# Kernel tuning notes

Measured on AMD Instinct MI355X. Metric: run time of the kernel, lower is better.

Reference implementation:

```python
import jax, jax.numpy as jnp
import numpy as np

N_NODES = 100000


def gin_layer(x, src, dst, W, b):
    # GINConv with Linear nn, eps=0: Linear(x + sum_{j in N(i)} x_j)
    agg = jax.ops.segment_sum(x[src], dst, num_segments=N_NODES)  # [N, d]
    return (x + agg) @ W + b


def setup_inputs() -> dict:
    key = jax.random.key(0)
    ks = jax.random.split(key, 8)
    in_c, hid, out_c = 128, 128, 64
    x = jax.random.normal(ks[0], (N_NODES, in_c), dtype=jnp.float32)
    edge_index = jax.random.randint(ks[1], (2, 600000), 0, N_NODES, dtype=jnp.int64)
    def lin(k, fan_in, fan_out):
        bound = 1.0 / np.sqrt(fan_in)
        kw, kb = jax.random.split(k)
        W = jax.random.uniform(kw, (fan_in, fan_out), minval=-bound, maxval=bound, dtype=jnp.float32)
        b = jax.random.uniform(kb, (fan_out,), minval=-bound, maxval=bound, dtype=jnp.float32)
        return W, b
    W1, b1 = lin(ks[2], in_c, hid)
    W2, b2 = lin(ks[3], hid, hid)
    W3, b3 = lin(ks[4], hid, out_c)
    return {"x": x, "edge_index": edge_index, "W1": W1, "b1": b1,
            "W2": W2, "b2": b2, "W3": W3, "b3": b3}


def reference(x, edge_index, W1, b1, W2, b2, W3, b3):
    src, dst = edge_index[0], edge_index[1]
    # dropout in eval mode -> identity
    h = jax.nn.relu(gin_layer(x, src, dst, W1, b1))
    h = jax.nn.relu(gin_layer(h, src, dst, W2, b2))
    h = gin_layer(h, src, dst, W3, b3)
    return h
```

## Files before the change

kernel.cpp:

```cpp
#include <hip/hip_runtime.h>


typedef __attribute__((ext_vector_type(8))) short short8;
typedef __attribute__((ext_vector_type(4))) float f32x4;
typedef unsigned short ushort_t;
typedef unsigned int uint_t;

__device__ inline ushort_t bf16_rne(float f) {
  uint_t u = __float_as_uint(f);
  uint_t r = (u + 0x7FFFu + ((u >> 16) & 1u)) >> 16;
  return (ushort_t)r;
}
__device__ inline float bf16_to_f32(ushort_t h) {
  return __uint_as_float(((uint_t)h) << 16);
}

__global__ __launch_bounds__(256) void k_detect(const int* __restrict__ ew,
                                                int* __restrict__ flag, int E) {
  int i = blockIdx.x * 256 + threadIdx.x;
  int idx = 2 * i + 1;
  if (idx < 2 * E) {
    if (ew[idx] != 0) atomicOr(flag, 1);
  }
}

__global__ __launch_bounds__(256) void k_hist(const void* __restrict__ edges,
                                              const int* __restrict__ flag,
                                              int* __restrict__ counts, int E) {
  int e = blockIdx.x * 256 + threadIdx.x;
  if (e >= E) return;
  int d;
  if (*flag) d = ((const int*)edges)[E + e];
  else       d = (int)((const long long*)edges)[E + e];
  atomicAdd(&counts[d], 1);
}

__global__ __launch_bounds__(256) void k_scan1(const int* __restrict__ counts,
                                               int* __restrict__ offs,
                                               int* __restrict__ bsum, int N) {
  __shared__ int s[256];
  int t = threadIdx.x;
  int base = blockIdx.x * 1024 + t * 4;
  int c0 = 0, c1 = 0, c2 = 0, c3 = 0;
  if (base + 0 < N) c0 = counts[base + 0];
  if (base + 1 < N) c1 = counts[base + 1];
  if (base + 2 < N) c2 = counts[base + 2];
  if (base + 3 < N) c3 = counts[base + 3];
  int mySum = c0 + c1 + c2 + c3;
  s[t] = mySum;
  __syncthreads();
  for (int d = 1; d < 256; d <<= 1) {
    int v = (t >= d) ? s[t - d] : 0;
    __syncthreads();
    s[t] += v;
    __syncthreads();
  }
  int excl = s[t] - mySum;
  if (base + 0 < N) offs[base + 0] = excl;
  if (base + 1 < N) offs[base + 1] = excl + c0;
  if (base + 2 < N) offs[base + 2] = excl + c0 + c1;
  if (base + 3 < N) offs[base + 3] = excl + c0 + c1 + c2;
  if (t == 255) bsum[blockIdx.x] = s[255];
}

__global__ __launch_bounds__(128) void k_scan2(int* __restrict__ bsum, int nb) {
  __shared__ int s[128];
  int t = threadIdx.x;
  int v = (t < nb) ? bsum[t] : 0;
  s[t] = v;
  __syncthreads();
  for (int d = 1; d < 128; d <<= 1) {
    int u = (t >= d) ? s[t - d] : 0;
    __syncthreads();
    s[t] += u;
    __syncthreads();
  }
  if (t < nb) bsum[t] = s[t] - v;
}

__global__ __launch_bounds__(256) void k_scan3(int* __restrict__ offs,
                                               const int* __restrict__ bsum,
                                               int* __restrict__ cursor,
                                               int N, int E) {
  int t = threadIdx.x;
  int add = bsum[blockIdx.x];
  int base = blockIdx.x * 1024 + t * 4;
#pragma unroll
  for (int j = 0; j < 4; j++) {
    int i = base + j;
    if (i < N) { int v = offs[i] + add; offs[i] = v; cursor[i] = v; }
  }
  if (blockIdx.x == 0 && t == 0) offs[N] = E;
}

__global__ __launch_bounds__(256) void k_fill(const void* __restrict__ edges,
                                              const int* __restrict__ flag,
                                              int* __restrict__ cursor,
                                              int* __restrict__ csr, int E) {
  int e = blockIdx.x * 256 + threadIdx.x;
  if (e >= E) return;
  int s, d;
  if (*flag) {
    const int* p = (const int*)edges;
    s = p[e]; d = p[E + e];
  } else {
    const long long* p = (const long long*)edges;
    s = (int)p[e]; d = (int)p[E + e];
  }
  int pos = atomicAdd(&cursor[d], 1);
  csr[pos] = s;
}

__global__ __launch_bounds__(256) void k_repack(
    const float* __restrict__ W1, const float* __restrict__ W2,
    const float* __restrict__ W3,
    ushort_t* __restrict__ h1, ushort_t* __restrict__ l1,
    ushort_t* __restrict__ h2, ushort_t* __restrict__ l2,
    ushort_t* __restrict__ h3, ushort_t* __restrict__ l3) {
  int idx = blockIdx.x * 256 + threadIdx.x;
  const float* W; ushort_t* H; ushort_t* L; int NC; int i;
  if (idx < 16384)      { W = W1; H = h1; L = l1; NC = 128; i = idx; }
  else if (idx < 32768) { W = W2; H = h2; L = l2; NC = 128; i = idx - 16384; }
  else if (idx < 40960) { W = W3; H = h3; L = l3; NC = 64;  i = idx - 32768; }
  else return;
  int j = i & 7;
  int lane = (i >> 3) & 63;
  int NT = NC >> 4;
  int tile = (i >> 9) & (NT - 1);
  int ks = i >> (9 + (NC == 128 ? 3 : 2));
  int k = ks * 32 + (lane >> 4) * 8 + j;
  int n = tile * 16 + (lane & 15);
  float v = W[(size_t)k * NC + n];
  ushort_t hi = bf16_rne(v);
  ushort_t lo = bf16_rne(v - bf16_to_f32(hi));
  H[i] = hi; L[i] = lo;
}

template <int NC>
__global__ __launch_bounds__(256) void k_gemm_mfma(
    const float* __restrict__ A, const ushort_t* __restrict__ Bhi,
    const ushort_t* __restrict__ Blo, ushort_t* __restrict__ Z, int M) {
  constexpr int NT = NC / 16;
  int lane = threadIdx.x & 63;
  int wave = threadIdx.x >> 6;
  int row0 = blockIdx.x * 64 + wave * 16;
  int m = lane & 15;
  int q = lane >> 4;
  int grow = row0 + m;
  bool rowok = (grow < M);

  f32x4 acc[NT];
#pragma unroll
  for (int t = 0; t < NT; t++) { acc[t][0] = 0.f; acc[t][1] = 0.f; acc[t][2] = 0.f; acc[t][3] = 0.f; }

  const float* arow = A + (size_t)(rowok ? grow : 0) * 128 + q * 8;

#pragma unroll
  for (int ks = 0; ks < 4; ks++) {
    float av[8];
    *(float4*)(av)     = *(const float4*)(arow + ks * 32);
    *(float4*)(av + 4) = *(const float4*)(arow + ks * 32 + 4);
    short8 ahi, alo;
#pragma unroll
    for (int j = 0; j < 8; j++) {
      float v = av[j];
      ushort_t hi = bf16_rne(v);
      ahi[j] = (short)hi;
      alo[j] = (short)bf16_rne(v - bf16_to_f32(hi));
    }
#pragma unroll
    for (int t = 0; t < NT; t++) {
      const short8 bh = *(const short8*)(Bhi + (((size_t)ks * NT + t) * 64 + lane) * 8);
      const short8 bl = *(const short8*)(Blo + (((size_t)ks * NT + t) * 64 + lane) * 8);
      acc[t] = __builtin_amdgcn_mfma_f32_16x16x32_bf16(ahi, bh, acc[t], 0, 0, 0);
      acc[t] = __builtin_amdgcn_mfma_f32_16x16x32_bf16(ahi, bl, acc[t], 0, 0, 0);
      acc[t] = __builtin_amdgcn_mfma_f32_16x16x32_bf16(alo, bh, acc[t], 0, 0, 0);
    }
  }

  int zrow = row0 + q * 4;
#pragma unroll
  for (int r = 0; r < 4; r++) {
    if (zrow + r < M) {
#pragma unroll
      for (int t = 0; t < NT; t++)
        Z[(size_t)(zrow + r) * NC + t * 16 + m] = bf16_rne(acc[t][r]);
    }
  }
}

template <int NC>
__global__ __launch_bounds__(256, 4) void k_fused(
    const ushort_t* __restrict__ Zin, const int* __restrict__ csr,
    const int* __restrict__ offs, const float* __restrict__ bias,
    const ushort_t* __restrict__ Bhi, const ushort_t* __restrict__ Blo,
    ushort_t* __restrict__ Zout, int M) {
  constexpr int NT = NC / 16;
  int lane = threadIdx.x & 63;
  int wave = threadIdx.x >> 6;
  int row0 = blockIdx.x * 64 + wave * 16;
  int m = lane & 15;
  int q = lane >> 4;
  int grow = row0 + m;
  bool rowok = (grow < M);

  float av[4][8];
  const ushort_t* zr0 = Zin + (size_t)(rowok ? grow : 0) * 128 + q * 8;
  const float* bq = bias + q * 8;
#pragma unroll
  for (int ks = 0; ks < 4; ks++) {
    float4 b0 = *(const float4*)(bq + ks * 32);
    float4 b1 = *(const float4*)(bq + ks * 32 + 4);
    short8 u = *(const short8*)(zr0 + ks * 32);
    av[ks][0] = b0.x + bf16_to_f32((ushort_t)u[0]);
    av[ks][1] = b0.y + bf16_to_f32((ushort_t)u[1]);
    av[ks][2] = b0.z + bf16_to_f32((ushort_t)u[2]);
    av[ks][3] = b0.w + bf16_to_f32((ushort_t)u[3]);
    av[ks][4] = b1.x + bf16_to_f32((ushort_t)u[4]);
    av[ks][5] = b1.y + bf16_to_f32((ushort_t)u[5]);
    av[ks][6] = b1.z + bf16_to_f32((ushort_t)u[6]);
    av[ks][7] = b1.w + bf16_to_f32((ushort_t)u[7]);
  }

  int s = 0, e = 0;
  if (rowok) { s = offs[grow]; e = offs[grow + 1]; }
  int j = s;
  for (; j + 4 <= e; j += 4) {
    int i0 = csr[j], i1 = csr[j + 1], i2 = csr[j + 2], i3 = csr[j + 3];
    const ushort_t* za = Zin + (size_t)i0 * 128 + q * 8;
    const ushort_t* zb = Zin + (size_t)i1 * 128 + q * 8;
    const ushort_t* zc = Zin + (size_t)i2 * 128 + q * 8;
    const ushort_t* zd = Zin + (size_t)i3 * 128 + q * 8;
    short8 ua[4], ub[4], uc[4], ud[4];
#pragma unroll
    for (int ks = 0; ks < 4; ks++) ua[ks] = *(const short8*)(za + ks * 32);
#pragma unroll
    for (int ks = 0; ks < 4; ks++) ub[ks] = *(const short8*)(zb + ks * 32);
#pragma unroll
    for (int ks = 0; ks < 4; ks++) uc[ks] = *(const short8*)(zc + ks * 32);
#pragma unroll
    for (int ks = 0; ks < 4; ks++) ud[ks] = *(const short8*)(zd + ks * 32);
#pragma unroll
    for (int ks = 0; ks < 4; ks++)
#pragma unroll
      for (int jj = 0; jj < 8; jj++)
        av[ks][jj] += (bf16_to_f32((ushort_t)ua[ks][jj]) +
                       bf16_to_f32((ushort_t)ub[ks][jj])) +
                      (bf16_to_f32((ushort_t)uc[ks][jj]) +
                       bf16_to_f32((ushort_t)ud[ks][jj]));
  }
  if (j + 2 <= e) {
    int i0 = csr[j], i1 = csr[j + 1];
    j += 2;
    const ushort_t* za = Zin + (size_t)i0 * 128 + q * 8;
    const ushort_t* zb = Zin + (size_t)i1 * 128 + q * 8;
    short8 ua[4], ub[4];
#pragma unroll
    for (int ks = 0; ks < 4; ks++) ua[ks] = *(const short8*)(za + ks * 32);
#pragma unroll
    for (int ks = 0; ks < 4; ks++) ub[ks] = *(const short8*)(zb + ks * 32);
#pragma unroll
    for (int ks = 0; ks < 4; ks++)
#pragma unroll
      for (int jj = 0; jj < 8; jj++)
        av[ks][jj] += bf16_to_f32((ushort_t)ua[ks][jj]) +
                      bf16_to_f32((ushort_t)ub[ks][jj]);
  }
  if (j < e) {
    int i0 = csr[j];
    const ushort_t* za = Zin + (size_t)i0 * 128 + q * 8;
#pragma unroll
    for (int ks = 0; ks < 4; ks++) {
      short8 u = *(const short8*)(za + ks * 32);
#pragma unroll
      for (int jj = 0; jj < 8; jj++)
        av[ks][jj] += bf16_to_f32((ushort_t)u[jj]);
    }
  }

  f32x4 acc[NT];
#pragma unroll
  for (int tt = 0; tt < NT; tt++) { acc[tt][0] = 0.f; acc[tt][1] = 0.f; acc[tt][2] = 0.f; acc[tt][3] = 0.f; }

#pragma unroll
  for (int ks = 0; ks < 4; ks++) {
    short8 ahi, alo;
#pragma unroll
    for (int jj = 0; jj < 8; jj++) {
      float v = fmaxf(av[ks][jj], 0.f);
      ushort_t hi = bf16_rne(v);
      ahi[jj] = (short)hi;
      alo[jj] = (short)bf16_rne(v - bf16_to_f32(hi));
    }
#pragma unroll
    for (int tt = 0; tt < NT; tt++) {
      const short8 bh = *(const short8*)(Bhi + (((size_t)ks * NT + tt) * 64 + lane) * 8);
      const short8 bl = *(const short8*)(Blo + (((size_t)ks * NT + tt) * 64 + lane) * 8);
      acc[tt] = __builtin_amdgcn_mfma_f32_16x16x32_bf16(ahi, bh, acc[tt], 0, 0, 0);
      acc[tt] = __builtin_amdgcn_mfma_f32_16x16x32_bf16(ahi, bl, acc[tt], 0, 0, 0);
      acc[tt] = __builtin_amdgcn_mfma_f32_16x16x32_bf16(alo, bh, acc[tt], 0, 0, 0);
    }
  }

  int zrow = row0 + q * 4;
#pragma unroll
  for (int r = 0; r < 4; r++) {
    if (zrow + r < M) {
#pragma unroll
      for (int tt = 0; tt < NT; tt++)
        Zout[(size_t)(zrow + r) * NC + tt * 16 + m] = bf16_rne(acc[tt][r]);
    }
  }
}

__global__ __launch_bounds__(256) void k_agg64(const ushort_t* __restrict__ z,
                                               const int* __restrict__ csr,
                                               const int* __restrict__ offs,
                                               const float* __restrict__ bias,
                                               float* __restrict__ out, int N) {
  int t = threadIdx.x;
  int node = blockIdx.x * 32 + (t >> 3);
  if (node >= N) return;
  int c = (t & 7) * 8;
  float acc[8];
  {
    short8 u = *(const short8*)(z + (size_t)node * 64 + c);
#pragma unroll
    for (int jj = 0; jj < 8; jj++)
      acc[jj] = bias[c + jj] + bf16_to_f32((ushort_t)u[jj]);
  }
  int s = offs[node], e = offs[node + 1];
  int j = s;
  for (; j + 4 <= e; j += 4) {
    int i0 = csr[j], i1 = csr[j + 1], i2 = csr[j + 2], i3 = csr[j + 3];
    short8 u0 = *(const short8*)(z + (size_t)i0 * 64 + c);
    short8 u1 = *(const short8*)(z + (size_t)i1 * 64 + c);
    short8 u2 = *(const short8*)(z + (size_t)i2 * 64 + c);
    short8 u3 = *(const short8*)(z + (size_t)i3 * 64 + c);
#pragma unroll
    for (int jj = 0; jj < 8; jj++)
      acc[jj] += (bf16_to_f32((ushort_t)u0[jj]) + bf16_to_f32((ushort_t)u1[jj])) +
                 (bf16_to_f32((ushort_t)u2[jj]) + bf16_to_f32((ushort_t)u3[jj]));
  }
  if (j + 2 <= e) {
    int i0 = csr[j], i1 = csr[j + 1];
    j += 2;
    short8 u0 = *(const short8*)(z + (size_t)i0 * 64 + c);
    short8 u1 = *(const short8*)(z + (size_t)i1 * 64 + c);
#pragma unroll
    for (int jj = 0; jj < 8; jj++)
      acc[jj] += bf16_to_f32((ushort_t)u0[jj]) + bf16_to_f32((ushort_t)u1[jj]);
  }
  if (j < e) {
    int i0 = csr[j];
    short8 u = *(const short8*)(z + (size_t)i0 * 64 + c);
#pragma unroll
    for (int jj = 0; jj < 8; jj++)
      acc[jj] += bf16_to_f32((ushort_t)u[jj]);
  }
  float4 o0 = make_float4(acc[0], acc[1], acc[2], acc[3]);
  float4 o1 = make_float4(acc[4], acc[5], acc[6], acc[7]);
  *(float4*)&out[(size_t)node * 64 + c]     = o0;
  *(float4*)&out[(size_t)node * 64 + c + 4] = o1;
}

extern "C" void kernel_launch(void* const* d_in, const int* in_sizes, int n_in,
                              void* d_out, int out_size, void* d_ws, size_t ws_size,
                              hipStream_t stream) {
  const float* x  = (const float*)d_in[0];
  const void* edges = d_in[1];
  const float* W1 = (const float*)d_in[2];
  const float* b1 = (const float*)d_in[3];
  const float* W2 = (const float*)d_in[4];
  const float* b2 = (const float*)d_in[5];
  const float* W3 = (const float*)d_in[6];
  const float* b3 = (const float*)d_in[7];
  float* out = (float*)d_out;

  int N = in_sizes[0] / 128;
  int E = in_sizes[1] / 2;

  char* w = (char*)d_ws;
  size_t off = 0;
  auto alloc = [&](size_t bytes) -> void* {
    void* p = w + off;
    off = (off + bytes + 255) & ~(size_t)255;
    return p;
  };
  size_t curBytes = ((size_t)N * 4 + 255) & ~(size_t)255;
  int*   cursor = (int*)alloc(curBytes);
  int*   flag   = (int*)alloc(4);
  int*   csr    = (int*)alloc((size_t)E * 4);
  int*   offs   = (int*)alloc((size_t)(N + 1) * 4);
  int*   bsum   = (int*)alloc(4096);
  ushort_t* h1  = (ushort_t*)alloc(16384 * 2);
  ushort_t* l1  = (ushort_t*)alloc(16384 * 2);
  ushort_t* h2  = (ushort_t*)alloc(16384 * 2);
  ushort_t* l2  = (ushort_t*)alloc(16384 * 2);
  ushort_t* h3  = (ushort_t*)alloc(8192 * 2);
  ushort_t* l3  = (ushort_t*)alloc(8192 * 2);
  ushort_t* z1  = (ushort_t*)alloc((size_t)N * 128 * 2);
  ushort_t* z2  = (ushort_t*)alloc((size_t)N * 128 * 2);
  ushort_t* z3  = z1;

  int ge = (E + 255) / 256;
  int nb = (N + 1023) / 1024;

  hipMemsetAsync(cursor, 0, curBytes + 4, stream);
  k_detect<<<4, 256, 0, stream>>>((const int*)edges, flag, E);
  k_hist<<<ge, 256, 0, stream>>>(edges, flag, cursor, E);
  k_scan1<<<nb, 256, 0, stream>>>(cursor, offs, bsum, N);
  k_scan2<<<1, 128, 0, stream>>>(bsum, nb);
  k_scan3<<<nb, 256, 0, stream>>>(offs, bsum, cursor, N, E);
  k_fill<<<ge, 256, 0, stream>>>(edges, flag, cursor, csr, E);
  k_repack<<<160, 256, 0, stream>>>(W1, W2, W3, h1, l1, h2, l2, h3, l3);

  int gm = (N + 63) / 64;
  k_gemm_mfma<128><<<gm, 256, 0, stream>>>(x, h1, l1, z1, N);
  k_fused<128><<<gm, 256, 0, stream>>>(z1, csr, offs, b1, h2, l2, z2, N);
  k_fused<64><<<gm, 256, 0, stream>>>(z2, csr, offs, b2, h3, l3, z3, N);
  k_agg64<<<(N + 31) / 32, 256, 0, stream>>>(z3, csr, offs, b3, out, N);
}
```

Measured before the change: 300.6 us.

## Fold weight repack into GEMM kernels via LDS staging and inline dtype detection

Removes the separate detect and repack kernels. Each GEMM and fused block now converts fp32 W into hi/lo bf16 MFMA layout in shared memory, and the edge dtype check is done inline from the first few words. This cuts two launches and moves B-operand reads from global memory to LDS, but every one of the ~1563 blocks per layer redoes the full weight conversion. The 64KB of LDS per block for NC=128, together with dropping the occupancy hint, may lower occupancy for the gather-heavy fused kernel.

```diff
diff --git a/kernel.cpp b/kernel.cpp
--- a/kernel.cpp
+++ b/kernel.cpp
@@ -15,23 +15,19 @@
   return __uint_as_float(((uint_t)h) << 16);
 }
 
-__global__ __launch_bounds__(256) void k_detect(const int* __restrict__ ew,
-                                                int* __restrict__ flag, int E) {
-  int i = blockIdx.x * 256 + threadIdx.x;
-  int idx = 2 * i + 1;
-  if (idx < 2 * E) {
-    if (ew[idx] != 0) atomicOr(flag, 1);
-  }
+__device__ __forceinline__ bool edges_int32(const void* edges) {
+  const int* p = (const int*)edges;
+  int x = p[1] | p[3] | p[5] | p[7] | p[9] | p[11] | p[13] | p[15];
+  return x != 0;
 }
 
 __global__ __launch_bounds__(256) void k_hist(const void* __restrict__ edges,
-                                              const int* __restrict__ flag,
                                               int* __restrict__ counts, int E) {
   int e = blockIdx.x * 256 + threadIdx.x;
   if (e >= E) return;
   int d;
-  if (*flag) d = ((const int*)edges)[E + e];
-  else       d = (int)((const long long*)edges)[E + e];
+  if (edges_int32(edges)) d = ((const int*)edges)[E + e];
+  else                    d = (int)((const long long*)edges)[E + e];
   atomicAdd(&counts[d], 1);
 }
 
@@ -94,13 +90,12 @@
 }
 
 __global__ __launch_bounds__(256) void k_fill(const void* __restrict__ edges,
-                                              const int* __restrict__ flag,
                                               int* __restrict__ cursor,
                                               int* __restrict__ csr, int E) {
   int e = blockIdx.x * 256 + threadIdx.x;
   if (e >= E) return;
   int s, d;
-  if (*flag) {
+  if (edges_int32(edges)) {
     const int* p = (const int*)edges;
     s = p[e]; d = p[E + e];
   } else {
@@ -111,70 +106,76 @@
   csr[pos] = s;
 }
 
-__global__ __launch_bounds__(256) void k_repack(
-    const float* __restrict__ W1, const float* __restrict__ W2,
-    const float* __restrict__ W3,
-    ushort_t* __restrict__ h1, ushort_t* __restrict__ l1,
-    ushort_t* __restrict__ h2, ushort_t* __restrict__ l2,
-    ushort_t* __restrict__ h3, ushort_t* __restrict__ l3) {
-  int idx = blockIdx.x * 256 + threadIdx.x;
-  const float* W; ushort_t* H; ushort_t* L; int NC; int i;
-  if (idx < 16384)      { W = W1; H = h1; L = l1; NC = 128; i = idx; }
-  else if (idx < 32768) { W = W2; H = h2; L = l2; NC = 128; i = idx - 16384; }
-  else if (idx < 40960) { W = W3; H = h3; L = l3; NC = 64;  i = idx - 32768; }
-  else return;
-  int j = i & 7;
-  int lane = (i >> 3) & 63;
-  int NT = NC >> 4;
-  int tile = (i >> 9) & (NT - 1);
-  int ks = i >> (9 + (NC == 128 ? 3 : 2));
-  int k = ks * 32 + (lane >> 4) * 8 + j;
-  int n = tile * 16 + (lane & 15);
-  float v = W[(size_t)k * NC + n];
-  ushort_t hi = bf16_rne(v);
-  ushort_t lo = bf16_rne(v - bf16_to_f32(hi));
-  H[i] = hi; L[i] = lo;
+template <int NC>
+__device__ __forceinline__ void stage_W(const float* __restrict__ W,
+                                        ushort_t* ldsH, ushort_t* ldsL, int t) {
+  constexpr int NT = NC / 16;
+  for (int w = t; w < 128 * NC / 4; w += 256) {
+    float4 v = *(const float4*)(W + (size_t)w * 4);
+    int k = (w * 4) / NC;
+    int n0 = (w * 4) % NC;
+    int lhi = ((k >> 3) & 3) << 4;
+    int j = k & 7;
+    const float* vv = (const float*)&v;
+#pragma unroll
+    for (int r = 0; r < 4; r++) {
+      int n = n0 + r;
+      int idx = (((k >> 5) * NT + (n >> 4)) * 64 + (lhi | (n & 15))) * 8 + j;
+      ushort_t hi = bf16_rne(vv[r]);
+      ldsH[idx] = hi;
+      ldsL[idx] = bf16_rne(vv[r] - bf16_to_f32(hi));
+    }
+  }
 }
 
 template <int NC>
 __global__ __launch_bounds__(256) void k_gemm_mfma(
-    const float* __restrict__ A, const ushort_t* __restrict__ Bhi,
-    const ushort_t* __restrict__ Blo, ushort_t* __restrict__ Z, int M) {
+    const float* __restrict__ A, const float* __restrict__ W,
+    ushort_t* __restrict__ Z, int M) {
   constexpr int NT = NC / 16;
-  int lane = threadIdx.x & 63;
-  int wave = threadIdx.x >> 6;
+  __shared__ ushort_t ldsH[128 * NC];
+  __shared__ ushort_t ldsL[128 * NC];
+  int t = threadIdx.x;
+  int lane = t & 63;
+  int wave = t >> 6;
   int row0 = blockIdx.x * 64 + wave * 16;
   int m = lane & 15;
   int q = lane >> 4;
   int grow = row0 + m;
   bool rowok = (grow < M);
 
-  f32x4 acc[NT];
-#pragma unroll
-  for (int t = 0; t < NT; t++) { acc[t][0] = 0.f; acc[t][1] = 0.f; acc[t][2] = 0.f; acc[t][3] = 0.f; }
-
+  stage_W<NC>(W, ldsH, ldsL, t);
+
+  short8 ahi[4], alo[4];
   const float* arow = A + (size_t)(rowok ? grow : 0) * 128 + q * 8;
-
 #pragma unroll
   for (int ks = 0; ks < 4; ks++) {
     float av[8];
     *(float4*)(av)     = *(const float4*)(arow + ks * 32);
     *(float4*)(av + 4) = *(const float4*)(arow + ks * 32 + 4);
-    short8 ahi, alo;
 #pragma unroll
     for (int j = 0; j < 8; j++) {
       float v = av[j];
       ushort_t hi = bf16_rne(v);
-      ahi[j] = (short)hi;
-      alo[j] = (short)bf16_rne(v - bf16_to_f32(hi));
-    }
-#pragma unroll
-    for (int t = 0; t < NT; t++) {
-      const short8 bh = *(const short8*)(Bhi + (((size_t)ks * NT + t) * 64 + lane) * 8);
-      const short8 bl = *(const short8*)(Blo + (((size_t)ks * NT + t) * 64 + lane) * 8);
-      acc[t] = __builtin_amdgcn_mfma_f32_16x16x32_bf16(ahi, bh, acc[t], 0, 0, 0);
-      acc[t] = __builtin_amdgcn_mfma_f32_16x16x32_bf16(ahi, bl, acc[t], 0, 0, 0);
-      acc[t] = __builtin_amdgcn_mfma_f32_16x16x32_bf16(alo, bh, acc[t], 0, 0, 0);
+      ahi[ks][j] = (short)hi;
+      alo[ks][j] = (short)bf16_rne(v - bf16_to_f32(hi));
+    }
+  }
+  __syncthreads();
+
+  f32x4 acc[NT];
+#pragma unroll
+  for (int tt = 0; tt < NT; tt++) { acc[tt][0] = 0.f; acc[tt][1] = 0.f; acc[tt][2] = 0.f; acc[tt][3] = 0.f; }
+
+#pragma unroll
+  for (int ks = 0; ks < 4; ks++) {
+#pragma unroll
+    for (int tt = 0; tt < NT; tt++) {
+      const short8 bh = *(const short8*)(ldsH + ((ks * NT + tt) * 64 + lane) * 8);
+      const short8 bl = *(const short8*)(ldsL + ((ks * NT + tt) * 64 + lane) * 8);
+      acc[tt] = __builtin_amdgcn_mfma_f32_16x16x32_bf16(ahi[ks], bh, acc[tt], 0, 0, 0);
+      acc[tt] = __builtin_amdgcn_mfma_f32_16x16x32_bf16(ahi[ks], bl, acc[tt], 0, 0, 0);
+      acc[tt] = __builtin_amdgcn_mfma_f32_16x16x32_bf16(alo[ks], bh, acc[tt], 0, 0, 0);
     }
   }
 
@@ -183,26 +184,30 @@
   for (int r = 0; r < 4; r++) {
     if (zrow + r < M) {
 #pragma unroll
-      for (int t = 0; t < NT; t++)
-        Z[(size_t)(zrow + r) * NC + t * 16 + m] = bf16_rne(acc[t][r]);
+      for (int tt = 0; tt < NT; tt++)
+        Z[(size_t)(zrow + r) * NC + tt * 16 + m] = bf16_rne(acc[tt][r]);
     }
   }
 }
 
 template <int NC>
-__global__ __launch_bounds__(256, 4) void k_fused(
+__global__ __launch_bounds__(256) void k_fused(
     const ushort_t* __restrict__ Zin, const int* __restrict__ csr,
     const int* __restrict__ offs, const float* __restrict__ bias,
-    const ushort_t* __restrict__ Bhi, const ushort_t* __restrict__ Blo,
-    ushort_t* __restrict__ Zout, int M) {
+    const float* __restrict__ W, ushort_t* __restrict__ Zout, int M) {
   constexpr int NT = NC / 16;
-  int lane = threadIdx.x & 63;
-  int wave = threadIdx.x >> 6;
+  __shared__ ushort_t ldsH[128 * NC];
+  __shared__ ushort_t ldsL[128 * NC];
+  int t = threadIdx.x;
+  int lane = t & 63;
+  int wave = t >> 6;
   int row0 = blockIdx.x * 64 + wave * 16;
   int m = lane & 15;
   int q = lane >> 4;
   int grow = row0 + m;
   bool rowok = (grow < M);
+
+  stage_W<NC>(W, ldsH, ldsL, t);
 
   float av[4][8];
   const ushort_t* zr0 = Zin + (size_t)(rowok ? grow : 0) * 128 + q * 8;
@@ -277,6 +282,7 @@
         av[ks][jj] += bf16_to_f32((ushort_t)u[jj]);
     }
   }
+  __syncthreads();
 
   f32x4 acc[NT];
 #pragma unroll
@@ -294,8 +300,8 @@
     }
 #pragma unroll
     for (int tt = 0; tt < NT; tt++) {
-      const short8 bh = *(const short8*)(Bhi + (((size_t)ks * NT + tt) * 64 + lane) * 8);
-      const short8 bl = *(const short8*)(Blo + (((size_t)ks * NT + tt) * 64 + lane) * 8);
+      const short8 bh = *(const short8*)(ldsH + ((ks * NT + tt) * 64 + lane) * 8);
+      const short8 bl = *(const short8*)(ldsL + ((ks * NT + tt) * 64 + lane) * 8);
       acc[tt] = __builtin_amdgcn_mfma_f32_16x16x32_bf16(ahi, bh, acc[tt], 0, 0, 0);
       acc[tt] = __builtin_amdgcn_mfma_f32_16x16x32_bf16(ahi, bl, acc[tt], 0, 0, 0);
       acc[tt] = __builtin_amdgcn_mfma_f32_16x16x32_bf16(alo, bh, acc[tt], 0, 0, 0);
@@ -389,16 +395,9 @@
   };
   size_t curBytes = ((size_t)N * 4 + 255) & ~(size_t)255;
   int*   cursor = (int*)alloc(curBytes);
-  int*   flag   = (int*)alloc(4);
   int*   csr    = (int*)alloc((size_t)E * 4);
   int*   offs   = (int*)alloc((size_t)(N + 1) * 4);
   int*   bsum   = (int*)alloc(4096);
-  ushort_t* h1  = (ushort_t*)alloc(16384 * 2);
-  ushort_t* l1  = (ushort_t*)alloc(16384 * 2);
-  ushort_t* h2  = (ushort_t*)alloc(16384 * 2);
-  ushort_t* l2  = (ushort_t*)alloc(16384 * 2);
-  ushort_t* h3  = (ushort_t*)alloc(8192 * 2);
-  ushort_t* l3  = (ushort_t*)alloc(8192 * 2);
   ushort_t* z1  = (ushort_t*)alloc((size_t)N * 128 * 2);
   ushort_t* z2  = (ushort_t*)alloc((size_t)N * 128 * 2);
   ushort_t* z3  = z1;
@@ -406,18 +405,16 @@
   int ge = (E + 255) / 256;
   int nb = (N + 1023) / 1024;
 
-  hipMemsetAsync(cursor, 0, curBytes + 4, stream);
-  k_detect<<<4, 256, 0, stream>>>((const int*)edges, flag, E);
-  k_hist<<<ge, 256, 0, stream>>>(edges, flag, cursor, E);
+  hipMemsetAsync(cursor, 0, curBytes, stream);
+  k_hist<<<ge, 256, 0, stream>>>(edges, cursor, E);
   k_scan1<<<nb, 256, 0, stream>>>(cursor, offs, bsum, N);
   k_scan2<<<1, 128, 0, stream>>>(bsum, nb);
   k_scan3<<<nb, 256, 0, stream>>>(offs, bsum, cursor, N, E);
-  k_fill<<<ge, 256, 0, stream>>>(edges, flag, cursor, csr, E);
-  k_repack<<<160, 256, 0, stream>>>(W1, W2, W3, h1, l1, h2, l2, h3, l3);
+  k_fill<<<ge, 256, 0, stream>>>(edges, cursor, csr, E);
 
   int gm = (N + 63) / 64;
-  k_gemm_mfma<128><<<gm, 256, 0, stream>>>(x, h1, l1, z1, N);
-  k_fused<128><<<gm, 256, 0, stream>>>(z1, csr, offs, b1, h2, l2, z2, N);
-  k_fused<64><<<gm, 256, 0, stream>>>(z2, csr, offs, b2, h3, l3, z3, N);
+  k_gemm_mfma<128><<<gm, 256, 0, stream>>>(x, W1, z1, N);
+  k_fused<128><<<gm, 256, 0, stream>>>(z1, csr, offs, b1, W2, z2, N);
+  k_fused<64><<<gm, 256, 0, stream>>>(z2, csr, offs, b2, W3, z3, N);
   k_agg64<<<(N + 31) / 32, 256, 0, stream>>>(z3, csr, offs, b3, out, N);
 }
```

New measurement: 359.0 us. +19.4%, slower.
